# Optimization experiments

Hardware: AMD Instinct MI355X
Metric: run time of the kernel (lower is better)

Reference implementation:

```python
import jax, jax.numpy as jnp
import numpy as np

H = 512  # hidden_size


def setup_inputs() -> dict:
    key = jax.random.key(0)
    ks = jax.random.split(key, 8)
    B, L = 16, 2048
    query = jax.random.normal(ks[0], (B, 1, 2 * H), dtype=jnp.float32)
    keys = jax.random.normal(ks[1], (B, L, 2 * H), dtype=jnp.float32)
    coverage = jax.random.uniform(ks[2], (B, L, 1), dtype=jnp.float32)
    # alignment MLP: Linear(4H+1 -> 2H, bias) -> tanh -> Linear(2H -> 1, no bias) -> softmax(dim=1)
    s1 = 1.0 / np.sqrt(4 * H + 1)
    W1 = jax.random.uniform(ks[3], (4 * H + 1, 2 * H), jnp.float32, -s1, s1)
    b1 = jax.random.uniform(ks[4], (2 * H,), jnp.float32, -s1, s1)
    s2 = 1.0 / np.sqrt(2 * H)
    W2 = jax.random.uniform(ks[5], (2 * H, 1), jnp.float32, -s2, s2)
    # reduce: Linear(2H -> H, no bias)
    Wr = jax.random.uniform(ks[6], (2 * H, H), jnp.float32, -s2, s2)
    return {"query": query, "keys": keys, "coverage": coverage,
            "W1": W1, "b1": b1, "W2": W2, "Wr": Wr}


def reference(query, keys, coverage, W1, b1, W2, Wr):
    B, L, _ = keys.shape
    q = jnp.broadcast_to(query, (B, L, query.shape[-1]))          # (B,L,2H)
    feat = jnp.concatenate([q, keys, coverage], axis=-1)          # (B,L,4H+1)
    h = jnp.tanh(feat @ W1 + b1)                                  # (B,L,2H)
    scores = h @ W2                                               # (B,L,1)
    attention = jax.nn.softmax(scores, axis=1)                    # softmax over length
    reduced = keys @ Wr                                           # (B,L,H)
    context = jnp.einsum('blo,blh->boh', attention, reduced)      # (B,1,H)
    return context, attention
```

## Files before the change

### kernel.cpp

```cpp
#include <hip/hip_runtime.h>
#include <hip/hip_bf16.h>
#include <stdint.h>

typedef short bf16x8 __attribute__((ext_vector_type(8)));
typedef float f32x4 __attribute__((ext_vector_type(4)));
typedef unsigned int u32x2 __attribute__((ext_vector_type(2)));

__device__ __forceinline__ uint32_t pack2f(float lo, float hi) {
  union { __hip_bfloat162 h; uint32_t u; } c;
  c.h.x = __float2bfloat16(lo);
  c.h.y = __float2bfloat16(hi);
  return c.u;
}

__device__ __forceinline__ unsigned short f32_to_bf16(float f) {
  union { __hip_bfloat16 h; unsigned short u; } c;
  c.h = __float2bfloat16(f);
  return c.u;
}

__device__ __forceinline__ float fast_tanh(float x) {
  float e = __builtin_amdgcn_exp2f(x * 2.8853900817779268f);
  return 1.0f - 2.0f * __builtin_amdgcn_rcpf(e + 1.0f);
}

#define GLD16(g, l)                                                                    \
  __builtin_amdgcn_global_load_lds((const __attribute__((address_space(1))) void*)(g), \
                                   (__attribute__((address_space(3))) void*)(l), 16, 0, 0)

__global__ void transpose_w1k(const float* __restrict__ W1, unsigned short* __restrict__ W1kt) {
  __shared__ float t[64][65];
  const int kb = blockIdx.x * 64;
  const int jb = blockIdx.y * 64;
  const int c = threadIdx.x & 63;
  const int r = threadIdx.x >> 6;
#pragma unroll
  for (int i = 0; i < 16; ++i) {
    const int k = i * 4 + r;
    t[k][c] = W1[(size_t)(1024 + kb + k) * 1024 + (jb + c)];
  }
  __syncthreads();
#pragma unroll
  for (int i = 0; i < 16; ++i) {
    const int j = i * 4 + r;
    W1kt[(size_t)(jb + j) * 1024 + (kb + c)] = f32_to_bf16(t[c][j]);
  }
}

__global__ void qterm_kernel(const float* __restrict__ query, const float* __restrict__ W1,
                             const float* __restrict__ b1, float* __restrict__ qterm) {
  const int b = blockIdx.y;
  const int j = blockIdx.x * 64 + (threadIdx.x & 63);
  const int kq = threadIdx.x >> 6;
  __shared__ float part[4][64];
  const float* q = query + b * 1024 + kq * 256;
  const float* wp = W1 + (size_t)(kq * 256) * 1024 + j;
  float acc = 0.f;
#pragma unroll 8
  for (int k = 0; k < 256; ++k) acc += q[k] * wp[(size_t)k * 1024];
  part[kq][threadIdx.x & 63] = acc;
  __syncthreads();
  if (threadIdx.x < 64) {
    const int jj = blockIdx.x * 64 + threadIdx.x;
    qterm[b * 1024 + jj] = b1[jj] + part[0][threadIdx.x] + part[1][threadIdx.x] +
                           part[2][threadIdx.x] + part[3][threadIdx.x];
  }
}

#define MFMA16(a, b, c) __builtin_amdgcn_mfma_f32_16x16x32_bf16(a, b, c, 0, 0, 0)
#define SBAR0() __builtin_amdgcn_sched_barrier(0)

#define STAGE_B(t, Bdst)                                          \
  _Pragma("unroll") for (int i = 0; i < 4; ++i) {                 \
    const int r = w * 32 + i * 8 + (lane >> 3);                   \
    const int u = (lane & 7) ^ (r & 7);                           \
    GLD16(W1kt + (((size_t)(col0 + r)) << 10) + (t) * 64 + u * 8, \
          (Bdst) + w * 4096 + lane * 16 + i * 1024);              \
  }

#define LOAD_A(t)                               \
  _Pragma("unroll") for (int j = 0; j < 8; ++j) \
      Ar[j] = *(const f32x4*)(gA + (t) * 64 + (size_t)j * 16 * 1024);

#define WRITE_A()                                                     \
  _Pragma("unroll") for (int j = 0; j < 8; ++j) {                     \
    const int r = arow + j * 16;                                      \
    u32x2 p;                                                          \
    p.x = pack2f(Ar[j].x, Ar[j].y);                                   \
    p.y = pack2f(Ar[j].z, Ar[j].w);                                   \
    *(u32x2*)(Alds + r * 128 + (((aun ^ (r & 7)) << 4) + auh)) = p;   \
  }

#define COMPUTE(Bsrc)                                                                        \
  _Pragma("unroll") for (int kk = 0; kk < 2; ++kk) {                                         \
    bf16x8 af[4], bfv[4];                                                                    \
    _Pragma("unroll") for (int mf = 0; mf < 4; ++mf) {                                       \
      const int ra = wm * 64 + mf * 16 + c16;                                                \
      af[mf] = *(const bf16x8*)(Alds + ra * 128 + (((kk * 4 + q4) ^ (ra & 7)) << 4));        \
    }                                                                                        \
    _Pragma("unroll") for (int nf = 0; nf < 4; ++nf) {                                       \
      const int ca = wn * 64 + nf * 16 + c16;                                                \
      bfv[nf] = *(const bf16x8*)((Bsrc) + ca * 128 + (((kk * 4 + q4) ^ (ca & 7)) << 4));     \
    }                                                                                        \
    _Pragma("unroll") for (int nf = 0; nf < 4; ++nf)                                         \
        _Pragma("unroll") for (int mf = 0; mf < 4; ++mf) acc[mf][nf] =                       \
            MFMA16(af[mf], bfv[nf], acc[mf][nf]);                                            \
  }

#define DRAIN_BAR()                                                   \
  asm volatile("s_waitcnt vmcnt(0) lgkmcnt(0)" ::: "memory");         \
  __builtin_amdgcn_s_barrier();

#define LGKM_BAR()                                                    \
  asm volatile("s_waitcnt lgkmcnt(0)" ::: "memory");                  \
  __builtin_amdgcn_s_barrier();

#define PIPE_ITER(t, Bc, Bn)          \
  if ((t) < 15) { STAGE_B((t) + 1, Bn); } \
  SBAR0();                            \
  COMPUTE(Bc);                        \
  if ((t) < 15) {                     \
    DRAIN_BAR();                      \
    WRITE_A();                        \
    if ((t) < 14) LOAD_A((t) + 2);    \
    LGKM_BAR();                       \
  }

__global__ __launch_bounds__(256, 3) void gemm_score_kernel(
    const float* __restrict__ keys, const unsigned short* __restrict__ W1kt,
    const float* __restrict__ qterm, const float* __restrict__ coverage,
    const float* __restrict__ W1, const float* __restrict__ W2,
    float* __restrict__ scores_part) {
  __shared__ __align__(16) unsigned char lds[50176];
  unsigned char* Alds = lds;
  unsigned char* B0 = lds + 16384;
  unsigned char* B1 = lds + 32768;
  float* Sred = (float*)(lds + 49152);

  const int tid = threadIdx.x;
  const int bid = blockIdx.x;
  const int xcd = bid & 7;
  const int idx = bid >> 3;
  const int rowgrp = xcd * 32 + (idx >> 3);
  const int colgrp = idx & 7;
  const int row0 = rowgrp * 128;
  const int col0 = colgrp * 128;
  const int b = row0 >> 11;
  const int w = tid >> 6;
  const int wm = w >> 1, wn = w & 1;
  const int lane = tid & 63;
  const int c16 = lane & 15, q4 = lane >> 4;

  const int arow = tid >> 4;
  const int akf = (tid & 15) * 4;
  const float* gA = keys + (size_t)(row0 + arow) * 1024 + akf;
  const int auh = (tid & 1) * 8;
  const int aun = (tid & 15) >> 1;

  f32x4 acc[4][4];
  const f32x4 zz = {0.f, 0.f, 0.f, 0.f};
#pragma unroll
  for (int mf = 0; mf < 4; ++mf)
#pragma unroll
    for (int nf = 0; nf < 4; ++nf) acc[mf][nf] = zz;

  f32x4 Ar[8];

  LOAD_A(0);
  SBAR0();
  STAGE_B(0, B0);
  SBAR0();
  WRITE_A();
  LOAD_A(1);
  SBAR0();
  asm volatile("s_waitcnt vmcnt(8) lgkmcnt(0)" ::: "memory");
  __builtin_amdgcn_s_barrier();

#pragma unroll 1
  for (int th = 0; th < 8; ++th) {
    const int t0 = th * 2, t1 = th * 2 + 1;
    PIPE_ITER(t0, B0, B1);
    PIPE_ITER(t1, B1, B0);
  }

  float covv[4][4];
#pragma unroll
  for (int mf = 0; mf < 4; ++mf)
#pragma unroll
    for (int r = 0; r < 4; ++r)
      covv[mf][r] = coverage[row0 + wm * 64 + mf * 16 + q4 * 4 + r];

  float p_part[4][4];
#pragma unroll
  for (int mf = 0; mf < 4; ++mf)
#pragma unroll
    for (int r = 0; r < 4; ++r) p_part[mf][r] = 0.f;

#pragma unroll
  for (int nf = 0; nf < 4; ++nf) {
    const int col = col0 + wn * 64 + nf * 16 + c16;
    const float qt = qterm[b * 1024 + col];
    const float w1c = W1[(size_t)2048 * 1024 + col];
    const float w2 = W2[col];
#pragma unroll
    for (int mf = 0; mf < 4; ++mf)
#pragma unroll
      for (int r = 0; r < 4; ++r) {
        float v = acc[mf][nf][r] + qt + covv[mf][r] * w1c;
        p_part[mf][r] += fast_tanh(v) * w2;
      }
  }

#pragma unroll
  for (int mf = 0; mf < 4; ++mf)
#pragma unroll
    for (int r = 0; r < 4; ++r) {
      float p = p_part[mf][r];
      p += __shfl_xor(p, 1);
      p += __shfl_xor(p, 2);
      p += __shfl_xor(p, 4);
      p += __shfl_xor(p, 8);
      if (c16 == 0) Sred[w * 64 + mf * 16 + q4 * 4 + r] = p;
    }
  __syncthreads();
  if (tid < 128) {
    const int wmv = tid >> 6, j = tid & 63;
    float s = Sred[wmv * 128 + j] + Sred[wmv * 128 + 64 + j];
    scores_part[(size_t)colgrp * 32768 + row0 + tid] = s;
  }
}

__global__ void softmax_kernel(const float* __restrict__ sp, float* __restrict__ att) {
  const int b = blockIdx.x;
  const int tid = threadIdx.x;
  float* a = att + b * 2048;
  __shared__ float red[4];
  float mx = -1e30f;
  for (int l = tid; l < 2048; l += 256) {
    float v = 0.f;
#pragma unroll
    for (int g = 0; g < 8; ++g) v += sp[(size_t)g * 32768 + b * 2048 + l];
    a[l] = v;
    mx = fmaxf(mx, v);
  }
#pragma unroll
  for (int o = 1; o < 64; o <<= 1) mx = fmaxf(mx, __shfl_xor(mx, o));
  if ((tid & 63) == 0) red[tid >> 6] = mx;
  __syncthreads();
  mx = fmaxf(fmaxf(red[0], red[1]), fmaxf(red[2], red[3]));
  __syncthreads();
  float sum = 0.f;
  for (int l = tid; l < 2048; l += 256) {
    float e = __expf(a[l] - mx);
    a[l] = e;
    sum += e;
  }
#pragma unroll
  for (int o = 1; o < 64; o <<= 1) sum += __shfl_xor(sum, o);
  if ((tid & 63) == 0) red[tid >> 6] = sum;
  __syncthreads();
  sum = red[0] + red[1] + red[2] + red[3];
  const float inv = 1.0f / sum;
  for (int l = tid; l < 2048; l += 256) a[l] *= inv;
}

__global__ void ctxpre_kernel(const float* __restrict__ keys, const float* __restrict__ att,
                              float* __restrict__ ctx_part) {
  const int b = blockIdx.x;
  const int sl = blockIdx.y;
  const int tid = threadIdx.x;
  const float* ab = att + b * 2048 + sl * 128;
  const f32x4* kp = (const f32x4*)(keys + ((size_t)b * 2048 + sl * 128) * 1024) + tid;
  f32x4 acc = {0.f, 0.f, 0.f, 0.f};
#pragma unroll 4
  for (int l = 0; l < 128; ++l) acc += kp[(size_t)l * 256] * ab[l];
  *(f32x4*)(ctx_part + ((size_t)(sl * 16 + b)) * 1024 + tid * 4) = acc;
}

__global__ void ctxreduce_kernel(const float* __restrict__ ctx_part, float* __restrict__ ctx_pre) {
  const int i = blockIdx.x * 256 + threadIdx.x;
  const int b = i >> 10, j = i & 1023;
  float s = 0.f;
#pragma unroll
  for (int sl = 0; sl < 16; ++sl) s += ctx_part[((size_t)(sl * 16 + b)) * 1024 + j];
  ctx_pre[i] = s;
}

__global__ void context_kernel(const float* __restrict__ ctx_pre, const float* __restrict__ Wr,
                               float* __restrict__ out) {
  const int b = blockIdx.y;
  const int h = blockIdx.x * 64 + (threadIdx.x & 63);
  const int jq = threadIdx.x >> 6;
  __shared__ float part[4][64];
  const float* cp = ctx_pre + b * 1024 + jq * 256;
  const float* wp = Wr + (size_t)(jq * 256) * 512 + h;
  float acc = 0.f;
#pragma unroll 8
  for (int k = 0; k < 256; ++k) acc += cp[k] * wp[(size_t)k * 512];
  part[jq][threadIdx.x & 63] = acc;
  __syncthreads();
  if (threadIdx.x < 64)
    out[b * 512 + blockIdx.x * 64 + threadIdx.x] = part[0][threadIdx.x] + part[1][threadIdx.x] +
                                                   part[2][threadIdx.x] + part[3][threadIdx.x];
}

extern "C" void kernel_launch(void* const* d_in, const int* in_sizes, int n_in, void* d_out,
                              int out_size, void* d_ws, size_t ws_size, hipStream_t stream) {
  const float* query = (const float*)d_in[0];
  const float* keys = (const float*)d_in[1];
  const float* coverage = (const float*)d_in[2];
  const float* W1 = (const float*)d_in[3];
  const float* b1 = (const float*)d_in[4];
  const float* W2 = (const float*)d_in[5];
  const float* Wr = (const float*)d_in[6];
  float* out = (float*)d_out;
  char* ws = (char*)d_ws;

  float* scores_part = (float*)ws;
  float* ctx_part = (float*)ws;
  float* ctx_pre = (float*)(ws + 1048576);
  float* qterm = (float*)(ws + 1114112);
  unsigned short* W1kt = (unsigned short*)(ws + 1179648);

  float* context_out = out;
  float* att_out = out + 8192;

  transpose_w1k<<<dim3(16, 16), dim3(256), 0, stream>>>(W1, W1kt);
  qterm_kernel<<<dim3(16, 16), dim3(256), 0, stream>>>(query, W1, b1, qterm);
  gemm_score_kernel<<<dim3(2048), dim3(256), 0, stream>>>(keys, W1kt, qterm, coverage, W1, W2,
                                                          scores_part);
  softmax_kernel<<<dim3(16), dim3(256), 0, stream>>>(scores_part, att_out);
  ctxpre_kernel<<<dim3(16, 16), dim3(256), 0, stream>>>(keys, att_out, ctx_part);
  ctxreduce_kernel<<<dim3(64), dim3(256), 0, stream>>>(ctx_part, ctx_pre);
  context_kernel<<<dim3(8, 16), dim3(256), 0, stream>>>(ctx_pre, Wr, context_out);
}
```

Before: 160.5 us.

## Pre-convert keys to tiled bf16 and use 512-thread 128x256 score GEMM

```diff
diff --git a/kernel.cpp b/kernel.cpp
--- a/kernel.cpp
+++ b/kernel.cpp
@@ -27,6 +27,9 @@
 #define GLD16(g, l)                                                                    \
   __builtin_amdgcn_global_load_lds((const __attribute__((address_space(1))) void*)(g), \
                                    (__attribute__((address_space(3))) void*)(l), 16, 0, 0)
+
+#define MFMA16(a, b, c) __builtin_amdgcn_mfma_f32_16x16x32_bf16(a, b, c, 0, 0, 0)
+#define SBAR0() __builtin_amdgcn_sched_barrier(0)
 
 __global__ void transpose_w1k(const float* __restrict__ W1, unsigned short* __restrict__ W1kt) {
   __shared__ float t[64][65];
@@ -44,6 +47,27 @@
   for (int i = 0; i < 16; ++i) {
     const int j = i * 4 + r;
     W1kt[(size_t)(jb + j) * 1024 + (kb + c)] = f32_to_bf16(t[c][j]);
+  }
+}
+
+__global__ void convert_keys(const float* __restrict__ keys, unsigned short* __restrict__ keysbf) {
+  const int mt = blockIdx.x >> 3;
+  const int ktg = blockIdx.x & 7;
+  const int t = threadIdx.x;
+  const int u = t & 7;
+  const int rb = t >> 3;
+#pragma unroll
+  for (int kk = 0; kk < 4; ++kk) {
+    const int kt = ktg * 4 + kk;
+#pragma unroll
+    for (int p = 0; p < 4; ++p) {
+      const int r = rb + p * 32;
+      f32x4 v = *(const f32x4*)(keys + (size_t)(mt * 128 + r) * 1024 + kt * 32 + u * 4);
+      u32x2 w;
+      w.x = pack2f(v.x, v.y);
+      w.y = pack2f(v.z, v.w);
+      *(u32x2*)(keysbf + ((size_t)(mt * 32 + kt) * 128 + r) * 32 + u * 4) = w;
+    }
   }
 }
 
@@ -67,10 +91,133 @@
   }
 }
 
-#define MFMA16(a, b, c) __builtin_amdgcn_mfma_f32_16x16x32_bf16(a, b, c, 0, 0, 0)
-#define SBAR0() __builtin_amdgcn_sched_barrier(0)
-
-#define STAGE_B(t, Bdst)                                          \
+
+#define V9_STAGE(kt_, Ad, Bd)                                                       \
+  {                                                                                 \
+    GLD16(gAsrc + (size_t)(kt_) * 4096, (Ad) + tid * 16);                           \
+    _Pragma("unroll") for (int i = 0; i < 2; ++i) {                                 \
+      const int c = (i * 512 + tid) >> 2;                                           \
+      const int k2 = tid & 3;                                                       \
+      GLD16(W1kt + (size_t)(col0 + c) * 1024 + (kt_) * 32 + k2 * 8,                 \
+            (Bd) + (i * 512 + tid) * 16);                                           \
+    }                                                                               \
+  }
+
+#define V9_COMPUTE(Ab, Bb)                                                          \
+  {                                                                                 \
+    bf16x8 af[4], bv[4];                                                            \
+    _Pragma("unroll") for (int mf = 0; mf < 4; ++mf)                                \
+        af[mf] = *(const bf16x8*)((Ab) + (wm * 64 + mf * 16 + c16) * 64 + q4 * 16); \
+    _Pragma("unroll") for (int nf = 0; nf < 4; ++nf)                                \
+        bv[nf] = *(const bf16x8*)((Bb) + (wn * 64 + nf * 16 + c16) * 64 + q4 * 16); \
+    _Pragma("unroll") for (int nf = 0; nf < 4; ++nf)                                \
+        _Pragma("unroll") for (int mf = 0; mf < 4; ++mf) acc[mf][nf] =              \
+            MFMA16(af[mf], bv[nf], acc[mf][nf]);                                    \
+  }
+
+#define V9_ITER(kt_, Ac, Bc, An, Bn)                              \
+  if ((kt_) < 31) { V9_STAGE((kt_) + 1, An, Bn); }                \
+  SBAR0();                                                        \
+  V9_COMPUTE(Ac, Bc);                                             \
+  SBAR0();                                                        \
+  asm volatile("s_waitcnt vmcnt(0) lgkmcnt(0)" ::: "memory");     \
+  __builtin_amdgcn_s_barrier();
+
+__global__ __launch_bounds__(512, 6) void gemm_score_v9(
+    const unsigned short* __restrict__ keysbf, const unsigned short* __restrict__ W1kt,
+    const float* __restrict__ qterm, const float* __restrict__ coverage,
+    const float* __restrict__ W1, const float* __restrict__ W2,
+    float* __restrict__ scores_part) {
+  __shared__ __align__(16) unsigned char lds[51200];
+  unsigned char* A0 = lds;
+  unsigned char* A1 = lds + 8192;
+  unsigned char* B0 = lds + 16384;
+  unsigned char* B1 = lds + 32768;
+  float* Sred = (float*)(lds + 49152);
+
+  const int tid = threadIdx.x;
+  const int bid = blockIdx.x;
+  const int xcd = bid & 7;
+  const int idx = bid >> 3;
+  const int rowt = xcd * 32 + (idx >> 2);
+  const int colgrp = idx & 3;
+  const int row0 = rowt * 128;
+  const int col0 = colgrp * 256;
+  const int b = row0 >> 11;
+  const int w = tid >> 6;
+  const int wm = w >> 2, wn = w & 3;
+  const int lane = tid & 63;
+  const int c16 = lane & 15, q4 = lane >> 4;
+
+  const unsigned short* gAsrc = keysbf + (size_t)(rowt * 32) * 4096 + tid * 8;
+
+  f32x4 acc[4][4];
+  const f32x4 zz = {0.f, 0.f, 0.f, 0.f};
+#pragma unroll
+  for (int mf = 0; mf < 4; ++mf)
+#pragma unroll
+    for (int nf = 0; nf < 4; ++nf) acc[mf][nf] = zz;
+
+  V9_STAGE(0, A0, B0);
+  asm volatile("s_waitcnt vmcnt(0)" ::: "memory");
+  __builtin_amdgcn_s_barrier();
+
+#pragma unroll 1
+  for (int th = 0; th < 16; ++th) {
+    const int t0 = th * 2, t1 = th * 2 + 1;
+    V9_ITER(t0, A0, B0, A1, B1);
+    V9_ITER(t1, A1, B1, A0, B0);
+  }
+
+  float covv[4][4];
+#pragma unroll
+  for (int mf = 0; mf < 4; ++mf)
+#pragma unroll
+    for (int r = 0; r < 4; ++r)
+      covv[mf][r] = coverage[row0 + wm * 64 + mf * 16 + q4 * 4 + r];
+
+  float p_part[4][4];
+#pragma unroll
+  for (int mf = 0; mf < 4; ++mf)
+#pragma unroll
+    for (int r = 0; r < 4; ++r) p_part[mf][r] = 0.f;
+
+#pragma unroll
+  for (int nf = 0; nf < 4; ++nf) {
+    const int col = col0 + wn * 64 + nf * 16 + c16;
+    const float qt = qterm[b * 1024 + col];
+    const float w1c = W1[(size_t)2048 * 1024 + col];
+    const float w2 = W2[col];
+#pragma unroll
+    for (int mf = 0; mf < 4; ++mf)
+#pragma unroll
+      for (int r = 0; r < 4; ++r) {
+        float v = acc[mf][nf][r] + qt + covv[mf][r] * w1c;
+        p_part[mf][r] += fast_tanh(v) * w2;
+      }
+  }
+
+#pragma unroll
+  for (int mf = 0; mf < 4; ++mf)
+#pragma unroll
+    for (int r = 0; r < 4; ++r) {
+      float p = p_part[mf][r];
+      p += __shfl_xor(p, 1);
+      p += __shfl_xor(p, 2);
+      p += __shfl_xor(p, 4);
+      p += __shfl_xor(p, 8);
+      if (c16 == 0) Sred[w * 64 + mf * 16 + q4 * 4 + r] = p;
+    }
+  __syncthreads();
+  if (tid < 128) {
+    const int wmv = tid >> 6, j = tid & 63;
+    float s = Sred[(wmv * 4 + 0) * 64 + j] + Sred[(wmv * 4 + 1) * 64 + j] +
+              Sred[(wmv * 4 + 2) * 64 + j] + Sred[(wmv * 4 + 3) * 64 + j];
+    scores_part[(size_t)colgrp * 32768 + row0 + tid] = s;
+  }
+}
+
+#define O8_STAGE_B(t, Bdst)                                       \
   _Pragma("unroll") for (int i = 0; i < 4; ++i) {                 \
     const int r = w * 32 + i * 8 + (lane >> 3);                   \
     const int u = (lane & 7) ^ (r & 7);                           \
@@ -78,55 +225,55 @@
           (Bdst) + w * 4096 + lane * 16 + i * 1024);              \
   }
 
-#define LOAD_A(t)                               \
+#define O8_LOAD_A(t)                            \
   _Pragma("unroll") for (int j = 0; j < 8; ++j) \
       Ar[j] = *(const f32x4*)(gA + (t) * 64 + (size_t)j * 16 * 1024);
 
-#define WRITE_A()                                                     \
-  _Pragma("unroll") for (int j = 0; j < 8; ++j) {                     \
-    const int r = arow + j * 16;                                      \
-    u32x2 p;                                                          \
-    p.x = pack2f(Ar[j].x, Ar[j].y);                                   \
-    p.y = pack2f(Ar[j].z, Ar[j].w);                                   \
-    *(u32x2*)(Alds + r * 128 + (((aun ^ (r & 7)) << 4) + auh)) = p;   \
-  }
-
-#define COMPUTE(Bsrc)                                                                        \
-  _Pragma("unroll") for (int kk = 0; kk < 2; ++kk) {                                         \
-    bf16x8 af[4], bfv[4];                                                                    \
-    _Pragma("unroll") for (int mf = 0; mf < 4; ++mf) {                                       \
-      const int ra = wm * 64 + mf * 16 + c16;                                                \
-      af[mf] = *(const bf16x8*)(Alds + ra * 128 + (((kk * 4 + q4) ^ (ra & 7)) << 4));        \
-    }                                                                                        \
-    _Pragma("unroll") for (int nf = 0; nf < 4; ++nf) {                                       \
-      const int ca = wn * 64 + nf * 16 + c16;                                                \
-      bfv[nf] = *(const bf16x8*)((Bsrc) + ca * 128 + (((kk * 4 + q4) ^ (ca & 7)) << 4));     \
-    }                                                                                        \
-    _Pragma("unroll") for (int nf = 0; nf < 4; ++nf)                                         \
-        _Pragma("unroll") for (int mf = 0; mf < 4; ++mf) acc[mf][nf] =                       \
-            MFMA16(af[mf], bfv[nf], acc[mf][nf]);                                            \
-  }
-
-#define DRAIN_BAR()                                                   \
-  asm volatile("s_waitcnt vmcnt(0) lgkmcnt(0)" ::: "memory");         \
+#define O8_WRITE_A()                                                \
+  _Pragma("unroll") for (int j = 0; j < 8; ++j) {                   \
+    const int r = arow + j * 16;                                    \
+    u32x2 p;                                                        \
+    p.x = pack2f(Ar[j].x, Ar[j].y);                                 \
+    p.y = pack2f(Ar[j].z, Ar[j].w);                                 \
+    *(u32x2*)(Alds + r * 128 + (((aun ^ (r & 7)) << 4) + auh)) = p; \
+  }
+
+#define O8_COMPUTE(Bsrc)                                                                 \
+  _Pragma("unroll") for (int kk = 0; kk < 2; ++kk) {                                     \
+    bf16x8 af[4], bfv[4];                                                                \
+    _Pragma("unroll") for (int mf = 0; mf < 4; ++mf) {                                   \
+      const int ra = wm * 64 + mf * 16 + c16;                                            \
+      af[mf] = *(const bf16x8*)(Alds + ra * 128 + (((kk * 4 + q4) ^ (ra & 7)) << 4));    \
+    }                                                                                    \
+    _Pragma("unroll") for (int nf = 0; nf < 4; ++nf) {                                   \
+      const int ca = wn * 64 + nf * 16 + c16;                                            \
+      bfv[nf] = *(const bf16x8*)((Bsrc) + ca * 128 + (((kk * 4 + q4) ^ (ca & 7)) << 4)); \
+    }                                                                                    \
+    _Pragma("unroll") for (int nf = 0; nf < 4; ++nf)                                     \
+        _Pragma("unroll") for (int mf = 0; mf < 4; ++mf) acc[mf][nf] =                   \
+            MFMA16(af[mf], bfv[nf], acc[mf][nf]);                                        \
+  }
+
+#define O8_DRAIN_BAR()                                        \
+  asm volatile("s_waitcnt vmcnt(0) lgkmcnt(0)" ::: "memory"); \
   __builtin_amdgcn_s_barrier();
 
-#define LGKM_BAR()                                                    \
-  asm volatile("s_waitcnt lgkmcnt(0)" ::: "memory");                  \
+#define O8_LGKM_BAR()                                \
+  asm volatile("s_waitcnt lgkmcnt(0)" ::: "memory"); \
   __builtin_amdgcn_s_barrier();
 
-#define PIPE_ITER(t, Bc, Bn)          \
-  if ((t) < 15) { STAGE_B((t) + 1, Bn); } \
-  SBAR0();                            \
-  COMPUTE(Bc);                        \
-  if ((t) < 15) {                     \
-    DRAIN_BAR();                      \
-    WRITE_A();                        \
-    if ((t) < 14) LOAD_A((t) + 2);    \
-    LGKM_BAR();                       \
-  }
-
-__global__ __launch_bounds__(256, 3) void gemm_score_kernel(
+#define O8_PIPE_ITER(t, Bc, Bn)                 \
+  if ((t) < 15) { O8_STAGE_B((t) + 1, Bn); }    \
+  SBAR0();                                      \
+  O8_COMPUTE(Bc);                               \
+  if ((t) < 15) {                               \
+    O8_DRAIN_BAR();                             \
+    O8_WRITE_A();                               \
+    if ((t) < 14) O8_LOAD_A((t) + 2);           \
+    O8_LGKM_BAR();                              \
+  }
+
+__global__ __launch_bounds__(256, 3) void gemm_score_o8(
     const float* __restrict__ keys, const unsigned short* __restrict__ W1kt,
     const float* __restrict__ qterm, const float* __restrict__ coverage,
     const float* __restrict__ W1, const float* __restrict__ W2,
@@ -166,12 +313,12 @@
 
   f32x4 Ar[8];
 
-  LOAD_A(0);
+  O8_LOAD_A(0);
   SBAR0();
-  STAGE_B(0, B0);
+  O8_STAGE_B(0, B0);
   SBAR0();
-  WRITE_A();
-  LOAD_A(1);
+  O8_WRITE_A();
+  O8_LOAD_A(1);
   SBAR0();
   asm volatile("s_waitcnt vmcnt(8) lgkmcnt(0)" ::: "memory");
   __builtin_amdgcn_s_barrier();
@@ -179,8 +326,8 @@
 #pragma unroll 1
   for (int th = 0; th < 8; ++th) {
     const int t0 = th * 2, t1 = th * 2 + 1;
-    PIPE_ITER(t0, B0, B1);
-    PIPE_ITER(t1, B1, B0);
+    O8_PIPE_ITER(t0, B0, B1);
+    O8_PIPE_ITER(t1, B1, B0);
   }
 
   float covv[4][4];
@@ -230,7 +377,8 @@
   }
 }
 
-__global__ void softmax_kernel(const float* __restrict__ sp, float* __restrict__ att) {
+__global__ void softmax_kernel(const float* __restrict__ sp, float* __restrict__ att,
+                               int ngroups) {
   const int b = blockIdx.x;
   const int tid = threadIdx.x;
   float* a = att + b * 2048;
@@ -238,8 +386,7 @@
   float mx = -1e30f;
   for (int l = tid; l < 2048; l += 256) {
     float v = 0.f;
-#pragma unroll
-    for (int g = 0; g < 8; ++g) v += sp[(size_t)g * 32768 + b * 2048 + l];
+    for (int g = 0; g < ngroups; ++g) v += sp[(size_t)g * 32768 + b * 2048 + l];
     a[l] = v;
     mx = fmaxf(mx, v);
   }
@@ -321,15 +468,25 @@
   float* ctx_pre = (float*)(ws + 1048576);
   float* qterm = (float*)(ws + 1114112);
   unsigned short* W1kt = (unsigned short*)(ws + 1179648);
+  unsigned short* keysbf = (unsigned short*)(ws + 3276800);
+
+  const bool fast = ws_size >= (size_t)70500000;
 
   float* context_out = out;
   float* att_out = out + 8192;
 
   transpose_w1k<<<dim3(16, 16), dim3(256), 0, stream>>>(W1, W1kt);
   qterm_kernel<<<dim3(16, 16), dim3(256), 0, stream>>>(query, W1, b1, qterm);
-  gemm_score_kernel<<<dim3(2048), dim3(256), 0, stream>>>(keys, W1kt, qterm, coverage, W1, W2,
-                                                          scores_part);
-  softmax_kernel<<<dim3(16), dim3(256), 0, stream>>>(scores_part, att_out);
+  if (fast) {
+    convert_keys<<<dim3(2048), dim3(256), 0, stream>>>(keys, keysbf);
+    gemm_score_v9<<<dim3(1024), dim3(512), 0, stream>>>(keysbf, W1kt, qterm, coverage, W1, W2,
+                                                        scores_part);
+    softmax_kernel<<<dim3(16), dim3(256), 0, stream>>>(scores_part, att_out, 4);
+  } else {
+    gemm_score_o8<<<dim3(2048), dim3(256), 0, stream>>>(keys, W1kt, qterm, coverage, W1, W2,
+                                                        scores_part);
+    softmax_kernel<<<dim3(16), dim3(256), 0, stream>>>(scores_part, att_out, 8);
+  }
   ctxpre_kernel<<<dim3(16, 16), dim3(256), 0, stream>>>(keys, att_out, ctx_part);
   ctxreduce_kernel<<<dim3(64), dim3(256), 0, stream>>>(ctx_part, ctx_pre);
   context_kernel<<<dim3(8, 16), dim3(256), 0, stream>>>(ctx_pre, Wr, context_out);
```

Result: slower. 521.3 us (+224.8%).
